# Performance work log

Measured on AMD Instinct MI355X. Metric: run time of the kernel, lower is better.

The kernel has to match this reference:

```python
import math
import jax, jax.numpy as jnp
import numpy as np

L_MAX = 2
B, N, V, P, C, NK = 4, 4096, 4096, 16, 16, 4


def _cg(j1, m1, j2, m2, J, M):
    # Clebsch-Gordan coefficient <j1 m1; j2 m2 | J M> (Racah formula, integer j)
    if M != m1 + m2:
        return 0.0
    f = math.factorial
    pref = (2 * J + 1) * f(j1 + j2 - J) * f(j1 - j2 + J) * f(-j1 + j2 + J) / f(j1 + j2 + J + 1)
    pref *= f(J + M) * f(J - M) * f(j1 - m1) * f(j1 + m1) * f(j2 - m2) * f(j2 + m2)
    t_lo = max(0, j2 - J - m1, j1 + m2 - J)
    t_hi = min(j1 + j2 - J, j1 - m1, j2 + m2)
    s = 0.0
    for t in range(t_lo, t_hi + 1):
        s += (-1) ** t / (f(t) * f(j1 + j2 - J - t) * f(j1 - m1 - t) * f(j2 + m2 - t)
                          * f(J - j2 + m1 + t) * f(J - j1 - m2 + t))
    return math.sqrt(pref) * s


def _Q(J, l, k):
    # Q[M+J, m+l, n+k] = <l m; k n | J M>, shape [2J+1, 2l+1, 2k+1]
    Q = np.zeros((2 * J + 1, 2 * l + 1, 2 * k + 1), np.float32)
    for M in range(-J, J + 1):
        for m in range(-l, l + 1):
            n = M - m
            if -k <= n <= k:
                Q[M + J, m + l, n + k] = _cg(l, m, k, n, J, M)
    return jnp.asarray(Q)


def setup_inputs() -> dict:
    key = jax.random.key(0)
    ks = jax.random.split(key, 8)
    inp = {}
    for l in range(L_MAX + 1):
        inp[f"signal_{l}"] = jax.random.normal(ks[l], (B, N, 2 * l + 1, C), jnp.float32)
        inp[f"kernel_{l}"] = jax.random.normal(ks[3 + l], (B, V, P, 2 * l + 1, NK), jnp.float32)
    pn = jax.random.randint(ks[6], (B, V, P), 0, N)
    pb = jnp.broadcast_to(jnp.arange(B)[:, None, None], (B, V, P))
    inp["patches_idx"] = jnp.stack([pb, pn], axis=-1).astype(jnp.int64)  # [B,V,P,2]
    return inp


def _forward(signals, kernels, patches_idx):
    pb = patches_idx[..., 0]
    pn = patches_idx[..., 1]
    y = {k: [] for k in kernels}
    y_cg = []  # (l, k, ylk)
    for l in sorted(signals):
        sl = signals[l][pb, pn]  # gather_nd -> [B,V,P,2l+1,C]
        for k in sorted(kernels):
            ylk = jnp.einsum('bvpkn,bvpmc->bvmknc', kernels[k], sl)
            b, v, m, kd, n, c = ylk.shape
            ylk = ylk.reshape(b, v, m, kd, n * c)  # [B,V,2l+1,2k+1,NK*C]
            if l > 0:
                y_cg.append((l, k, ylk))
            else:
                y[k].append(ylk[:, :, 0, :, :])  # degree-k output [B,V,2k+1,NK*C]
    # Clebsch-Gordan decomposition of each l>0 pair into degrees J <= L_MAX
    for (l, k, ylk) in y_cg:
        for J in range(abs(l - k), min(l + k, L_MAX) + 1):
            Q = _Q(J, l, k)
            yJ = jnp.einsum('Jmn,bvmnc->bvJc', Q, ylk)
            y.setdefault(J, []).append(yJ)
    return tuple(jnp.concatenate(y[J], axis=-1) for J in sorted(y))


def reference(signal_0, signal_1, signal_2, kernel_0, kernel_1, kernel_2, patches_idx):
    signals = {0: signal_0, 1: signal_1, 2: signal_2}
    kernels = {0: kernel_0, 1: kernel_1, 2: kernel_2}
    return _forward(signals, kernels, patches_idx)
```

## Files before the change

### kernel.cpp

```cpp
#include <hip/hip_runtime.h>
#include <math.h>

#define V_DIM 4096
#define N_DIM 4096

__device__ inline double dfac(int x){ double r=1.0; for(int i=2;i<=x;++i) r*=(double)i; return r; }

__global__ void build_q_kernel(float* __restrict__ Qt){
  int tid = blockIdx.x*blockDim.x + threadIdx.x;
  if(tid >= 580) return;
  const int Lc[12]={1,1,1,1,1,1,2,2,2,2,2,2};
  const int Kc[12]={0,1,1,1,2,2,0,1,1,2,2,2};
  const int Jc[12]={1,0,1,2,1,2,2,1,2,0,1,2};
  const int SZ[12]={9,9,27,45,45,75,25,45,75,25,75,125};
  int ci=0, rem=tid;
  while(rem >= SZ[ci]){ rem -= SZ[ci]; ++ci; }
  const int l=Lc[ci], k=Kc[ci], J=Jc[ci];
  const int tk=2*k+1, tl=2*l+1;
  const int n = rem % tk - k;
  const int m = (rem / tk) % tl - l;
  const int M = rem / (tk*tl) - J;
  float val = 0.f;
  if(M == m+n){
    double pref = (double)(2*J+1) * dfac(l+k-J)*dfac(l-k+J)*dfac(-l+k+J)/dfac(l+k+J+1);
    pref *= dfac(J+M)*dfac(J-M)*dfac(l-m)*dfac(l+m)*dfac(k-n)*dfac(k+n);
    int tlo = max(0, max(k-J-m, l+n-J));
    int thi = min(l+k-J, min(l-m, k+n));
    double s = 0.0;
    for(int tt=tlo; tt<=thi; ++tt){
      double d = dfac(tt)*dfac(l+k-J-tt)*dfac(l-m-tt)*dfac(k+n-tt)*dfac(J-k+m+tt)*dfac(J-l-n+tt);
      s += ((tt&1)? -1.0 : 1.0)/d;
    }
    val = (float)(sqrt(pref)*s);
  }
  Qt[tid] = val;
}

__global__ void detect_kernel(const unsigned* __restrict__ pw, int* __restrict__ flag){
  unsigned acc = 0u;
  for(int i=0;i<32;++i) acc |= pw[2*i+1];
  *flag = (acc==0u) ? 2 : 1;
}


template<int L_, int K_, int J_, int OFF_, int W_, int CHOFF_>
__device__ __forceinline__ void cg_out(const float* __restrict__ Qt,
                                       const float (&y)[9][9],
                                       float* __restrict__ optr,
                                       size_t bvs, int t){
  constexpr int MGB = (L_==0)?0:((L_==1)?1:4);
  constexpr int KGB = (K_==0)?0:((K_==1)?1:4);
  #pragma unroll
  for(int M=-J_; M<=J_; ++M){
    float acc = 0.f;
    #pragma unroll
    for(int m=-L_; m<=L_; ++m){
      const int nn = M - m;
      if(nn < -K_ || nn > K_) continue;
      const float q = Qt[OFF_ + ((M+J_)*(2*L_+1) + (m+L_))*(2*K_+1) + (nn+K_)];
      acc += q * y[MGB + m + L_][KGB + nn + K_];
    }
    optr[(bvs*(2*J_+1) + (size_t)(M+J_))*W_ + CHOFF_ + t] = acc;
  }
}

__global__ __launch_bounds__(64)
void conv_kernel(const float* __restrict__ sig0, const float* __restrict__ ker0,
                 const float* __restrict__ sig1, const float* __restrict__ ker1,
                 const float* __restrict__ sig2, const float* __restrict__ ker2,
                 const unsigned* __restrict__ pw, const int* __restrict__ flag,
                 const float* __restrict__ Qt, float* __restrict__ out){
  __shared__ __align__(16) float sig_lds[16*144];
  __shared__ __align__(16) float kern_lds[16*9*4];
  __shared__ int pn_s[16], pb_s[16];

  const int t  = threadIdx.x;
  const int bv = blockIdx.x;
  const size_t bvs = (size_t)bv;

  if(t < 16){
    const int s = *flag;
    const size_t e = ((size_t)bv*16 + t)*2;
    pb_s[t] = (int)pw[(e+0)*s] & 3;
    pn_s[t] = (int)pw[(e+1)*s] & (N_DIM-1);
  }

  {
    const float4* s4 = (const float4*)(ker0 + bvs*16*1*4);
    for(int j=t; j<16; j+=64){ ((float4*)kern_lds)[j*9 + 0] = s4[j]; }
    s4 = (const float4*)(ker1 + bvs*16*3*4);
    for(int j=t; j<48; j+=64){ int p=j/3, kd=j%3; ((float4*)kern_lds)[p*9 + 1 + kd] = s4[j]; }
    s4 = (const float4*)(ker2 + bvs*16*5*4);
    for(int j=t; j<80; j+=64){ int p=j/5, kd=j%5; ((float4*)kern_lds)[p*9 + 4 + kd] = s4[j]; }
  }
  __syncthreads();

  for(int i=t; i<16*36; i+=64){
    const int p = i/36, r4 = i%36;
    const size_t row = (size_t)pb_s[p]*N_DIM + pn_s[p];
    float4 v4;
    if(r4 < 4)        v4 = ((const float4*)(sig0 + row*16))[r4];
    else if(r4 < 16)  v4 = ((const float4*)(sig1 + row*48))[r4-4];
    else              v4 = ((const float4*)(sig2 + row*80))[r4-16];
    ((float4*)sig_lds)[p*36 + r4] = v4;
  }
  __syncthreads();

  const int n = t >> 4, c = t & 15;
  float y[9][9];
  #pragma unroll
  for(int a=0;a<9;++a)
    #pragma unroll
    for(int b_=0;b_<9;++b_) y[a][b_] = 0.f;

  #pragma unroll
  for(int p=0;p<16;++p){
    float s[9], kk[9];
    #pragma unroll
    for(int m=0;m<9;++m)  s[m]  = sig_lds[p*144 + m*16 + c];
    #pragma unroll
    for(int kd=0;kd<9;++kd) kk[kd] = kern_lds[(p*9 + kd)*4 + n];
    #pragma unroll
    for(int m=0;m<9;++m)
      #pragma unroll
      for(int kd=0;kd<9;++kd) y[m][kd] += s[m]*kk[kd];
  }

  float* o0 = out;
  float* o1 = out + 3145728;
  float* o2 = out + 22020096;

  o0[bvs*192 + t] = y[0][0];
  #pragma unroll
  for(int kd=0;kd<3;++kd) o1[(bvs*3 + kd)*384 + t] = y[0][1+kd];
  #pragma unroll
  for(int kd=0;kd<5;++kd) o2[(bvs*5 + kd)*384 + t] = y[0][4+kd];

  cg_out<1,1,0,  9,192, 64>(Qt, y, o0, bvs, t);
  cg_out<2,2,0,355,192,128>(Qt, y, o0, bvs, t);
  cg_out<1,0,1,  0,384, 64>(Qt, y, o1, bvs, t);
  cg_out<1,1,1, 18,384,128>(Qt, y, o1, bvs, t);
  cg_out<1,2,1, 90,384,192>(Qt, y, o1, bvs, t);
  cg_out<2,1,1,235,384,256>(Qt, y, o1, bvs, t);
  cg_out<2,2,1,380,384,320>(Qt, y, o1, bvs, t);
  cg_out<1,1,2, 45,384, 64>(Qt, y, o2, bvs, t);
  cg_out<1,2,2,135,384,128>(Qt, y, o2, bvs, t);
  cg_out<2,0,2,210,384,192>(Qt, y, o2, bvs, t);
  cg_out<2,1,2,280,384,256>(Qt, y, o2, bvs, t);
  cg_out<2,2,2,455,384,320>(Qt, y, o2, bvs, t);
}

extern "C" void kernel_launch(void* const* d_in, const int* in_sizes, int n_in,
                              void* d_out, int out_size, void* d_ws, size_t ws_size,
                              hipStream_t stream) {
  const float *s0=nullptr,*s1=nullptr,*s2=nullptr,*k0=nullptr,*k1=nullptr,*k2=nullptr;
  const void* pidx=nullptr;
  if(n_in >= 7){
    s0=(const float*)d_in[0]; k0=(const float*)d_in[1];
    s1=(const float*)d_in[2]; k1=(const float*)d_in[3];
    s2=(const float*)d_in[4]; k2=(const float*)d_in[5];
    pidx=d_in[6];
  }
  for(int i=0;i<n_in;++i){
    switch(in_sizes[i]){
      case 262144:  s0=(const float*)d_in[i]; break;
      case 786432:  s1=(const float*)d_in[i]; break;
      case 1310720: s2=(const float*)d_in[i]; break;
      case 1048576: k0=(const float*)d_in[i]; break;
      case 3145728: k1=(const float*)d_in[i]; break;
      case 5242880: k2=(const float*)d_in[i]; break;
      case 524288:  pidx=d_in[i]; break;
      default: break;
    }
  }

  float* Qt  = (float*)d_ws;
  int* flag  = (int*)((char*)d_ws + 4096);

  build_q_kernel<<<3, 256, 0, stream>>>(Qt);
  detect_kernel<<<1, 1, 0, stream>>>((const unsigned*)pidx, flag);
  conv_kernel<<<16384, 64, 0, stream>>>(s0, k0, s1, k1, s2, k2,
                                        (const unsigned*)pidx, flag, Qt,
                                        (float*)d_out);
}
```

Before: 311.7 us.

## Merge setup kernels, transpose kernel LDS layout, and unroll signal gather

Folds the Q-table build and index-format detection into a single setup launch, which removes one kernel launch. The per-patch kernel weights are stored transposed in LDS so each thread reads its nine kernel values with two float4 loads plus one scalar load instead of nine strided scalar loads. The signal gather now gives each thread a fixed patch and quarter-row, with an unrolled loop and no per-iteration division or branching. The main kernel is still dominated by output writes, so the gain is expected to be small.

```diff
diff --git a/kernel.cpp b/kernel.cpp
--- a/kernel.cpp
+++ b/kernel.cpp
@@ -6,8 +6,16 @@
 
 __device__ inline double dfac(int x){ double r=1.0; for(int i=2;i<=x;++i) r*=(double)i; return r; }
 
-__global__ void build_q_kernel(float* __restrict__ Qt){
-  int tid = blockIdx.x*blockDim.x + threadIdx.x;
+__global__ void setup_kernel(float* __restrict__ Qt,
+                             const unsigned* __restrict__ pw,
+                             int* __restrict__ flag){
+  const int tid = threadIdx.x;
+  if(tid == 1016){
+    unsigned acc = 0u;
+    for(int i=0;i<32;++i) acc |= pw[2*i+1];
+    *flag = (acc==0u) ? 2 : 1;
+    return;
+  }
   if(tid >= 580) return;
   const int Lc[12]={1,1,1,1,1,1,2,2,2,2,2,2};
   const int Kc[12]={0,1,1,1,2,2,0,1,1,2,2,2};
@@ -36,12 +44,6 @@
   Qt[tid] = val;
 }
 
-__global__ void detect_kernel(const unsigned* __restrict__ pw, int* __restrict__ flag){
-  unsigned acc = 0u;
-  for(int i=0;i<32;++i) acc |= pw[2*i+1];
-  *flag = (acc==0u) ? 2 : 1;
-}
-
 
 template<int L_, int K_, int J_, int OFF_, int W_, int CHOFF_>
 __device__ __forceinline__ void cg_out(const float* __restrict__ Qt,
@@ -71,7 +73,7 @@
                  const unsigned* __restrict__ pw, const int* __restrict__ flag,
                  const float* __restrict__ Qt, float* __restrict__ out){
   __shared__ __align__(16) float sig_lds[16*144];
-  __shared__ __align__(16) float kern_lds[16*9*4];
+  __shared__ __align__(16) float kern_t[16*48];
   __shared__ int pn_s[16], pb_s[16];
 
   const int t  = threadIdx.x;
@@ -86,23 +88,39 @@
   }
 
   {
-    const float4* s4 = (const float4*)(ker0 + bvs*16*1*4);
-    for(int j=t; j<16; j+=64){ ((float4*)kern_lds)[j*9 + 0] = s4[j]; }
-    s4 = (const float4*)(ker1 + bvs*16*3*4);
-    for(int j=t; j<48; j+=64){ int p=j/3, kd=j%3; ((float4*)kern_lds)[p*9 + 1 + kd] = s4[j]; }
-    s4 = (const float4*)(ker2 + bvs*16*5*4);
-    for(int j=t; j<80; j+=64){ int p=j/5, kd=j%5; ((float4*)kern_lds)[p*9 + 4 + kd] = s4[j]; }
+    if(t < 16){
+      float4 v = ((const float4*)(ker0 + bvs*64))[t];
+      float* d = &kern_t[t*48];
+      d[0*12+0]=v.x; d[1*12+0]=v.y; d[2*12+0]=v.z; d[3*12+0]=v.w;
+    }
+    if(t < 48){
+      float4 v = ((const float4*)(ker1 + bvs*192))[t];
+      int p = t/3, kd = t%3;
+      float* d = &kern_t[p*48 + 1 + kd];
+      d[0*12]=v.x; d[1*12]=v.y; d[2*12]=v.z; d[3*12]=v.w;
+    }
+    #pragma unroll
+    for(int j=t; j<80; j+=64){
+      float4 v = ((const float4*)(ker2 + bvs*320))[j];
+      int p = j/5, kd = j%5;
+      float* d = &kern_t[p*48 + 4 + kd];
+      d[0*12]=v.x; d[1*12]=v.y; d[2*12]=v.z; d[3*12]=v.w;
+    }
   }
   __syncthreads();
 
-  for(int i=t; i<16*36; i+=64){
-    const int p = i/36, r4 = i%36;
+  {
+    const int p = t>>2, q = t&3;
     const size_t row = (size_t)pb_s[p]*N_DIM + pn_s[p];
-    float4 v4;
-    if(r4 < 4)        v4 = ((const float4*)(sig0 + row*16))[r4];
-    else if(r4 < 16)  v4 = ((const float4*)(sig1 + row*48))[r4-4];
-    else              v4 = ((const float4*)(sig2 + row*80))[r4-16];
-    ((float4*)sig_lds)[p*36 + r4] = v4;
+    const float4* r0 = (const float4*)(sig0 + row*16);
+    const float4* r1 = (const float4*)(sig1 + row*48);
+    const float4* r2 = (const float4*)(sig2 + row*80);
+    float4* dst = ((float4*)sig_lds) + p*36;
+    dst[q] = r0[q];
+    #pragma unroll
+    for(int j=1;j<4;++j)  dst[q+4*j] = r1[q+4*j-4];
+    #pragma unroll
+    for(int j=4;j<9;++j)  dst[q+4*j] = r2[q+4*j-16];
   }
   __syncthreads();
 
@@ -115,11 +133,17 @@
 
   #pragma unroll
   for(int p=0;p<16;++p){
-    float s[9], kk[9];
-    #pragma unroll
-    for(int m=0;m<9;++m)  s[m]  = sig_lds[p*144 + m*16 + c];
-    #pragma unroll
-    for(int kd=0;kd<9;++kd) kk[kd] = kern_lds[(p*9 + kd)*4 + n];
+    float kk[9];
+    {
+      float4 a = *(const float4*)&kern_t[p*48 + n*12];
+      float4 b = *(const float4*)&kern_t[p*48 + n*12 + 4];
+      kk[0]=a.x; kk[1]=a.y; kk[2]=a.z; kk[3]=a.w;
+      kk[4]=b.x; kk[5]=b.y; kk[6]=b.z; kk[7]=b.w;
+      kk[8]=kern_t[p*48 + n*12 + 8];
+    }
+    float s[9];
+    #pragma unroll
+    for(int m=0;m<9;++m)  s[m] = sig_lds[p*144 + m*16 + c];
     #pragma unroll
     for(int m=0;m<9;++m)
       #pragma unroll
@@ -174,11 +198,10 @@
     }
   }
 
-  float* Qt  = (float*)d_ws;
-  int* flag  = (int*)((char*)d_ws + 4096);
-
-  build_q_kernel<<<3, 256, 0, stream>>>(Qt);
-  detect_kernel<<<1, 1, 0, stream>>>((const unsigned*)pidx, flag);
+  float* Qt = (float*)d_ws;
+  int* flag = (int*)((char*)d_ws + 4096);
+
+  setup_kernel<<<1, 1024, 0, stream>>>(Qt, (const unsigned*)pidx, flag);
   conv_kernel<<<16384, 64, 0, stream>>>(s0, k0, s1, k1, s2, k2,
                                         (const unsigned*)pidx, flag, Qt,
                                         (float*)d_out);
```

New measurement: 289.2 us. 7.2% less time.

## Split CG products across four waves with compile-time Clebsch-Gordan tables

Applied to the files above, without the earlier changes.

Each block grows from one wavefront to four. The degree-pair products are spread across the waves so that each wave holds a smaller accumulator set, which cuts register pressure compared with the single 9x9 array. Clebsch-Gordan coefficients become constexpr tables folded into the code, which removes the Q-build and detect kernel launches and the global Qt loads. Index-width detection moves to a per-block wave ballot. Gather and kernel loads are also split across waves, at the cost of some load imbalance between the waves.

```diff
diff --git a/kernel.cpp b/kernel.cpp
--- a/kernel.cpp
+++ b/kernel.cpp
@@ -1,153 +1,214 @@
 #include <hip/hip_runtime.h>
-#include <math.h>
-
-#define V_DIM 4096
+
 #define N_DIM 4096
 
-__device__ inline double dfac(int x){ double r=1.0; for(int i=2;i<=x;++i) r*=(double)i; return r; }
-
-__global__ void build_q_kernel(float* __restrict__ Qt){
-  int tid = blockIdx.x*blockDim.x + threadIdx.x;
-  if(tid >= 580) return;
-  const int Lc[12]={1,1,1,1,1,1,2,2,2,2,2,2};
-  const int Kc[12]={0,1,1,1,2,2,0,1,1,2,2,2};
-  const int Jc[12]={1,0,1,2,1,2,2,1,2,0,1,2};
-  const int SZ[12]={9,9,27,45,45,75,25,45,75,25,75,125};
-  int ci=0, rem=tid;
-  while(rem >= SZ[ci]){ rem -= SZ[ci]; ++ci; }
-  const int l=Lc[ci], k=Kc[ci], J=Jc[ci];
-  const int tk=2*k+1, tl=2*l+1;
-  const int n = rem % tk - k;
-  const int m = (rem / tk) % tl - l;
-  const int M = rem / (tk*tl) - J;
-  float val = 0.f;
-  if(M == m+n){
-    double pref = (double)(2*J+1) * dfac(l+k-J)*dfac(l-k+J)*dfac(-l+k+J)/dfac(l+k+J+1);
-    pref *= dfac(J+M)*dfac(J-M)*dfac(l-m)*dfac(l+m)*dfac(k-n)*dfac(k+n);
-    int tlo = max(0, max(k-J-m, l+n-J));
-    int thi = min(l+k-J, min(l-m, k+n));
-    double s = 0.0;
-    for(int tt=tlo; tt<=thi; ++tt){
-      double d = dfac(tt)*dfac(l+k-J-tt)*dfac(l-m-tt)*dfac(k+n-tt)*dfac(J-k+m+tt)*dfac(J-l-n+tt);
-      s += ((tt&1)? -1.0 : 1.0)/d;
-    }
-    val = (float)(sqrt(pref)*s);
-  }
-  Qt[tid] = val;
-}
-
-__global__ void detect_kernel(const unsigned* __restrict__ pw, int* __restrict__ flag){
-  unsigned acc = 0u;
-  for(int i=0;i<32;++i) acc |= pw[2*i+1];
-  *flag = (acc==0u) ? 2 : 1;
-}
-
-
-template<int L_, int K_, int J_, int OFF_, int W_, int CHOFF_>
-__device__ __forceinline__ void cg_out(const float* __restrict__ Qt,
-                                       const float (&y)[9][9],
-                                       float* __restrict__ optr,
-                                       size_t bvs, int t){
-  constexpr int MGB = (L_==0)?0:((L_==1)?1:4);
-  constexpr int KGB = (K_==0)?0:((K_==1)?1:4);
+constexpr double cfac(int x){ double r=1.0; for(int i=2;i<=x;++i) r*=(double)i; return r; }
+constexpr double csqrt_(double x){ double g = x>1.0? x:1.0; for(int i=0;i<200;++i) g=0.5*(g+x/g); return g; }
+constexpr double cg_coef(int l,int m,int k,int n,int J,int M){
+  if(M != m+n) return 0.0;
+  if(n < -k || n > k) return 0.0;
+  double pref = (double)(2*J+1)*cfac(l+k-J)*cfac(l-k+J)*cfac(-l+k+J)/cfac(l+k+J+1);
+  pref *= cfac(J+M)*cfac(J-M)*cfac(l-m)*cfac(l+m)*cfac(k-n)*cfac(k+n);
+  int tlo = 0;
+  if(k-J-m > tlo) tlo = k-J-m;
+  if(l+n-J > tlo) tlo = l+n-J;
+  int thi = l+k-J;
+  if(l-m < thi) thi = l-m;
+  if(k+n < thi) thi = k+n;
+  double s = 0.0;
+  for(int t=tlo; t<=thi; ++t){
+    double d = cfac(t)*cfac(l+k-J-t)*cfac(l-m-t)*cfac(k+n-t)*cfac(J-k+m+t)*cfac(J-l-n+t);
+    s += ((t&1)? -1.0 : 1.0)/d;
+  }
+  return csqrt_(pref)*s;
+}
+
+template<int L_,int K_,int J_> struct QtabT { float a[2*J_+1][2*L_+1]; };
+template<int L_,int K_,int J_>
+constexpr QtabT<L_,K_,J_> make_q(){
+  QtabT<L_,K_,J_> q{};
+  for(int M=-J_;M<=J_;++M)
+    for(int m=-L_;m<=L_;++m)
+      q.a[M+J_][m+L_] = (float)cg_coef(L_,m,K_,M-m,J_,M);
+  return q;
+}
+
+template<int L_,int K_,int J_,int W_,int CHOFF_>
+__device__ __forceinline__ void cg_store(const float (&y)[2*L_+1][2*K_+1],
+                                         float* __restrict__ o, size_t bvs, int lane){
+  constexpr QtabT<L_,K_,J_> Q = make_q<L_,K_,J_>();
   #pragma unroll
-  for(int M=-J_; M<=J_; ++M){
+  for(int Mi=0; Mi<2*J_+1; ++Mi){
     float acc = 0.f;
     #pragma unroll
-    for(int m=-L_; m<=L_; ++m){
-      const int nn = M - m;
-      if(nn < -K_ || nn > K_) continue;
-      const float q = Qt[OFF_ + ((M+J_)*(2*L_+1) + (m+L_))*(2*K_+1) + (nn+K_)];
-      acc += q * y[MGB + m + L_][KGB + nn + K_];
-    }
-    optr[(bvs*(2*J_+1) + (size_t)(M+J_))*W_ + CHOFF_ + t] = acc;
-  }
-}
-
-__global__ __launch_bounds__(64)
+    for(int mi=0; mi<2*L_+1; ++mi){
+      const int ni = (Mi-J_) - (mi-L_) + K_;
+      if(ni < 0 || ni > 2*K_) continue;
+      acc += Q.a[Mi][mi] * y[mi][ni];
+    }
+    o[(bvs*(2*J_+1) + (size_t)Mi)*W_ + CHOFF_ + lane] = acc;
+  }
+}
+
+__global__ __launch_bounds__(256, 4)
 void conv_kernel(const float* __restrict__ sig0, const float* __restrict__ ker0,
                  const float* __restrict__ sig1, const float* __restrict__ ker1,
                  const float* __restrict__ sig2, const float* __restrict__ ker2,
-                 const unsigned* __restrict__ pw, const int* __restrict__ flag,
-                 const float* __restrict__ Qt, float* __restrict__ out){
+                 const unsigned* __restrict__ pw, float* __restrict__ out){
   __shared__ __align__(16) float sig_lds[16*144];
-  __shared__ __align__(16) float kern_lds[16*9*4];
-  __shared__ int pn_s[16], pb_s[16];
-
-  const int t  = threadIdx.x;
-  const int bv = blockIdx.x;
+  __shared__ __align__(16) float kern_t[16*48];
+
+  const int t    = threadIdx.x;
+  const int w    = t >> 6;
+  const int lane = t & 63;
+  const int bv   = blockIdx.x;
   const size_t bvs = (size_t)bv;
-
-  if(t < 16){
-    const int s = *flag;
-    const size_t e = ((size_t)bv*16 + t)*2;
-    pb_s[t] = (int)pw[(e+0)*s] & 3;
-    pn_s[t] = (int)pw[(e+1)*s] & (N_DIM-1);
-  }
-
+  const int n = lane >> 4, c = lane & 15;
+
+  int row = 0;
   {
-    const float4* s4 = (const float4*)(ker0 + bvs*16*1*4);
-    for(int j=t; j<16; j+=64){ ((float4*)kern_lds)[j*9 + 0] = s4[j]; }
-    s4 = (const float4*)(ker1 + bvs*16*3*4);
-    for(int j=t; j<48; j+=64){ int p=j/3, kd=j%3; ((float4*)kern_lds)[p*9 + 1 + kd] = s4[j]; }
-    s4 = (const float4*)(ker2 + bvs*16*5*4);
-    for(int j=t; j<80; j+=64){ int p=j/5, kd=j%5; ((float4*)kern_lds)[p*9 + 4 + kd] = s4[j]; }
+    const unsigned probe = (lane < 16) ? pw[2*lane + 1] : 0u;
+    const unsigned long long nz = __ballot(probe != 0u);
+    const size_t s = (nz == 0ull) ? 2 : 1;
+    if(lane < 16){
+      const size_t e = ((size_t)bv*16 + lane)*2;
+      const int pb = (int)pw[(e+0)*s] & 3;
+      const int pn = (int)pw[(e+1)*s] & (N_DIM-1);
+      row = pb*N_DIM + pn;
+    }
+  }
+
+  if(w == 3){
+    if(lane < 16){
+      float4 v = ((const float4*)(ker0 + bvs*64))[lane];
+      float* d = &kern_t[lane*48];
+      d[0]=v.x; d[12]=v.y; d[24]=v.z; d[36]=v.w;
+    }
+    if(lane < 48){
+      float4 v = ((const float4*)(ker1 + bvs*192))[lane];
+      const int p = lane/3, kd = lane%3;
+      float* d = &kern_t[p*48 + 1 + kd];
+      d[0]=v.x; d[12]=v.y; d[24]=v.z; d[36]=v.w;
+    }
+    for(int j=lane; j<80; j+=64){
+      float4 v = ((const float4*)(ker2 + bvs*320))[j];
+      const int p = j/5, kd = j%5;
+      float* d = &kern_t[p*48 + 4 + kd];
+      d[0]=v.x; d[12]=v.y; d[24]=v.z; d[36]=v.w;
+    }
+  } else {
+    const int p = lane >> 2, q = lane & 3;
+    const size_t ro = (size_t)__shfl(row, p);
+    float4* dst = ((float4*)sig_lds) + p*36;
+    if(w == 0){
+      dst[q]    = ((const float4*)(sig0 + ro*16))[q];
+      dst[q+4]  = ((const float4*)(sig1 + ro*48))[q];
+      dst[q+8]  = ((const float4*)(sig1 + ro*48))[q+4];
+    } else if(w == 1){
+      dst[q+12] = ((const float4*)(sig1 + ro*48))[q+8];
+      dst[q+16] = ((const float4*)(sig2 + ro*80))[q];
+      dst[q+20] = ((const float4*)(sig2 + ro*80))[q+4];
+    } else {
+      dst[q+24] = ((const float4*)(sig2 + ro*80))[q+8];
+      dst[q+28] = ((const float4*)(sig2 + ro*80))[q+12];
+      dst[q+32] = ((const float4*)(sig2 + ro*80))[q+16];
+    }
   }
   __syncthreads();
-
-  for(int i=t; i<16*36; i+=64){
-    const int p = i/36, r4 = i%36;
-    const size_t row = (size_t)pb_s[p]*N_DIM + pn_s[p];
-    float4 v4;
-    if(r4 < 4)        v4 = ((const float4*)(sig0 + row*16))[r4];
-    else if(r4 < 16)  v4 = ((const float4*)(sig1 + row*48))[r4-4];
-    else              v4 = ((const float4*)(sig2 + row*80))[r4-16];
-    ((float4*)sig_lds)[p*36 + r4] = v4;
-  }
-  __syncthreads();
-
-  const int n = t >> 4, c = t & 15;
-  float y[9][9];
-  #pragma unroll
-  for(int a=0;a<9;++a)
-    #pragma unroll
-    for(int b_=0;b_<9;++b_) y[a][b_] = 0.f;
-
-  #pragma unroll
-  for(int p=0;p<16;++p){
-    float s[9], kk[9];
-    #pragma unroll
-    for(int m=0;m<9;++m)  s[m]  = sig_lds[p*144 + m*16 + c];
-    #pragma unroll
-    for(int kd=0;kd<9;++kd) kk[kd] = kern_lds[(p*9 + kd)*4 + n];
-    #pragma unroll
-    for(int m=0;m<9;++m)
-      #pragma unroll
-      for(int kd=0;kd<9;++kd) y[m][kd] += s[m]*kk[kd];
-  }
 
   float* o0 = out;
   float* o1 = out + 3145728;
   float* o2 = out + 22020096;
 
-  o0[bvs*192 + t] = y[0][0];
-  #pragma unroll
-  for(int kd=0;kd<3;++kd) o1[(bvs*3 + kd)*384 + t] = y[0][1+kd];
-  #pragma unroll
-  for(int kd=0;kd<5;++kd) o2[(bvs*5 + kd)*384 + t] = y[0][4+kd];
-
-  cg_out<1,1,0,  9,192, 64>(Qt, y, o0, bvs, t);
-  cg_out<2,2,0,355,192,128>(Qt, y, o0, bvs, t);
-  cg_out<1,0,1,  0,384, 64>(Qt, y, o1, bvs, t);
-  cg_out<1,1,1, 18,384,128>(Qt, y, o1, bvs, t);
-  cg_out<1,2,1, 90,384,192>(Qt, y, o1, bvs, t);
-  cg_out<2,1,1,235,384,256>(Qt, y, o1, bvs, t);
-  cg_out<2,2,1,380,384,320>(Qt, y, o1, bvs, t);
-  cg_out<1,1,2, 45,384, 64>(Qt, y, o2, bvs, t);
-  cg_out<1,2,2,135,384,128>(Qt, y, o2, bvs, t);
-  cg_out<2,0,2,210,384,192>(Qt, y, o2, bvs, t);
-  cg_out<2,1,2,280,384,256>(Qt, y, o2, bvs, t);
-  cg_out<2,2,2,455,384,320>(Qt, y, o2, bvs, t);
+  if(w == 0){
+    float y[5][5] = {};
+    #pragma unroll
+    for(int p=0;p<16;++p){
+      float s[5], kk[5];
+      #pragma unroll
+      for(int i=0;i<5;++i) s[i] = sig_lds[p*144 + (4+i)*16 + c];
+      float4 a = *(const float4*)&kern_t[p*48 + n*12 + 4];
+      kk[0]=a.x; kk[1]=a.y; kk[2]=a.z; kk[3]=a.w; kk[4]=kern_t[p*48 + n*12 + 8];
+      #pragma unroll
+      for(int i=0;i<5;++i)
+        #pragma unroll
+        for(int j=0;j<5;++j) y[i][j] += s[i]*kk[j];
+    }
+    cg_store<2,2,0,192,128>(y, o0, bvs, lane);
+    cg_store<2,2,1,384,320>(y, o1, bvs, lane);
+    cg_store<2,2,2,384,320>(y, o2, bvs, lane);
+  } else if(w == 1){
+    float y0[1][5] = {}, y1[3][5] = {};
+    #pragma unroll
+    for(int p=0;p<16;++p){
+      float s0v = sig_lds[p*144 + c];
+      float s[3], kk[5];
+      #pragma unroll
+      for(int i=0;i<3;++i) s[i] = sig_lds[p*144 + (1+i)*16 + c];
+      float4 a = *(const float4*)&kern_t[p*48 + n*12 + 4];
+      kk[0]=a.x; kk[1]=a.y; kk[2]=a.z; kk[3]=a.w; kk[4]=kern_t[p*48 + n*12 + 8];
+      #pragma unroll
+      for(int j=0;j<5;++j){
+        y0[0][j] += s0v*kk[j];
+        #pragma unroll
+        for(int i=0;i<3;++i) y1[i][j] += s[i]*kk[j];
+      }
+    }
+    #pragma unroll
+    for(int kd=0;kd<5;++kd) o2[(bvs*5 + kd)*384 + lane] = y0[0][kd];
+    cg_store<1,2,1,384,192>(y1, o1, bvs, lane);
+    cg_store<1,2,2,384,128>(y1, o2, bvs, lane);
+  } else if(w == 2){
+    float y11[3][3] = {}, y21[5][3] = {};
+    #pragma unroll
+    for(int p=0;p<16;++p){
+      float s1[3], s2[5], kk[3];
+      #pragma unroll
+      for(int i=0;i<3;++i) s1[i] = sig_lds[p*144 + (1+i)*16 + c];
+      #pragma unroll
+      for(int i=0;i<5;++i) s2[i] = sig_lds[p*144 + (4+i)*16 + c];
+      #pragma unroll
+      for(int j=0;j<3;++j) kk[j] = kern_t[p*48 + n*12 + 1 + j];
+      #pragma unroll
+      for(int j=0;j<3;++j){
+        #pragma unroll
+        for(int i=0;i<3;++i) y11[i][j] += s1[i]*kk[j];
+        #pragma unroll
+        for(int i=0;i<5;++i) y21[i][j] += s2[i]*kk[j];
+      }
+    }
+    cg_store<1,1,0,192, 64>(y11, o0, bvs, lane);
+    cg_store<1,1,1,384,128>(y11, o1, bvs, lane);
+    cg_store<1,1,2,384, 64>(y11, o2, bvs, lane);
+    cg_store<2,1,1,384,256>(y21, o1, bvs, lane);
+    cg_store<2,1,2,384,256>(y21, o2, bvs, lane);
+  } else {
+    float y00 = 0.f, y01[3] = {};
+    float y10[3][1] = {}, y20[5][1] = {};
+    #pragma unroll
+    for(int p=0;p<16;++p){
+      float s0v = sig_lds[p*144 + c];
+      float sm[8];
+      #pragma unroll
+      for(int i=0;i<8;++i) sm[i] = sig_lds[p*144 + (1+i)*16 + c];
+      float k0v = kern_t[p*48 + n*12];
+      float k13[3];
+      #pragma unroll
+      for(int j=0;j<3;++j) k13[j] = kern_t[p*48 + n*12 + 1 + j];
+      y00 += s0v*k0v;
+      #pragma unroll
+      for(int j=0;j<3;++j) y01[j] += s0v*k13[j];
+      #pragma unroll
+      for(int i=0;i<3;++i) y10[i][0] += sm[i]*k0v;
+      #pragma unroll
+      for(int i=0;i<5;++i) y20[i][0] += sm[3+i]*k0v;
+    }
+    o0[bvs*192 + lane] = y00;
+    #pragma unroll
+    for(int kd=0;kd<3;++kd) o1[(bvs*3 + kd)*384 + lane] = y01[kd];
+    cg_store<1,0,1,384, 64>(y10, o1, bvs, lane);
+    cg_store<2,0,2,384,192>(y20, o2, bvs, lane);
+  }
 }
 
 extern "C" void kernel_launch(void* const* d_in, const int* in_sizes, int n_in,
@@ -174,12 +235,6 @@
     }
   }
 
-  float* Qt  = (float*)d_ws;
-  int* flag  = (int*)((char*)d_ws + 4096);
-
-  build_q_kernel<<<3, 256, 0, stream>>>(Qt);
-  detect_kernel<<<1, 1, 0, stream>>>((const unsigned*)pidx, flag);
-  conv_kernel<<<16384, 64, 0, stream>>>(s0, k0, s1, k1, s2, k2,
-                                        (const unsigned*)pidx, flag, Qt,
-                                        (float*)d_out);
-}
+  conv_kernel<<<16384, 256, 0, stream>>>(s0, k0, s1, k1, s2, k2,
+                                         (const unsigned*)pidx, (float*)d_out);
+}
```

Result: faster. 288.7 us (-7.4%).
